# Performance work log

Measured on AMD Instinct MI355X. Metric: run time of the kernel, lower is better.

The kernel has to match this reference:

```python
import jax, jax.numpy as jnp
import numpy as np
from jax import lax

B = 32768
IMG = 28
K = 3
OUT_HW = IMG - K + 1  # 26
FLAT = OUT_HW * OUT_HW  # 676
HID = 300
NCLS = 10


def setup_inputs() -> dict:
    key = jax.random.key(0)
    ks = jax.random.split(key, 8)
    x = jax.random.normal(ks[0], (B, IMG * IMG), dtype=jnp.float32)
    conv_w = jax.random.normal(ks[1], (K, K), dtype=jnp.float32) * 0.1
    # Linear params stored as (in, out) so forward is h @ W + b
    W1 = jax.random.normal(ks[2], (FLAT, HID), dtype=jnp.float32) * 0.04
    b1 = jnp.zeros((HID,), dtype=jnp.float32)
    W2 = jax.random.normal(ks[3], (HID, HID), dtype=jnp.float32) * 0.06
    b2 = jnp.zeros((HID,), dtype=jnp.float32)
    W3 = jax.random.normal(ks[4], (HID, NCLS), dtype=jnp.float32) * 0.06
    b3 = jnp.zeros((NCLS,), dtype=jnp.float32)
    return {"x": x, "conv_w": conv_w, "W1": W1, "b1": b1,
            "W2": W2, "b2": b2, "W3": W3, "b3": b3}


def reference(x, conv_w, W1, b1, W2, b2, W3, b3):
    b = x.shape[0]
    img = x.reshape(b, 1, IMG, IMG)  # NCHW
    # Valid cross-correlation with 3x3 kernel -> [B,1,26,26]
    y = lax.conv_general_dilated(
        img, conv_w[None, None, :, :], window_strides=(1, 1), padding="VALID",
        dimension_numbers=("NCHW", "OIHW", "NCHW"))
    h = y.reshape(b, FLAT)
    h = jax.nn.relu(h @ W1 + b1)
    h = jax.nn.relu(h @ W2 + b2)
    return h @ W3 + b3
```

## Files before the change

kernel.cpp:

```cpp
#include <hip/hip_runtime.h>


typedef __bf16 bf16_t;
typedef __bf16 bf16x4 __attribute__((ext_vector_type(4)));
typedef __bf16 bf16x8 __attribute__((ext_vector_type(8)));
typedef float  f32x4  __attribute__((ext_vector_type(4)));

#define MFMA16(a, b, c) __builtin_amdgcn_mfma_f32_16x16x32_bf16((a), (b), (c), 0, 0, 0)

#define W1F_ELEMS (25 * 20 * 64 * 8)
#define W2F_ELEMS (10 * 20 * 64 * 8)
#define W3F_ELEMS (10 * 1 * 64 * 8)
#define ASTRIDE   136

#define W1F_GRP 32000
#define W2F_GRP 12800
#define W3F_GRP 640

#define WG_BARRIER_NODRAIN()                                   \
    do {                                                       \
        asm volatile("s_waitcnt lgkmcnt(0)" ::: "memory");     \
        __builtin_amdgcn_s_barrier();                          \
        __builtin_amdgcn_sched_barrier(0);                     \
    } while (0)

__global__ __launch_bounds__(256) void prep_weights(
    const float* __restrict__ conv_w, const float* __restrict__ W1,
    const float* __restrict__ W2, const float* __restrict__ W3,
    bf16x8* __restrict__ W1f, bf16x8* __restrict__ W2f,
    bf16x8* __restrict__ W3f) {
    int idx = blockIdx.x * 256 + threadIdx.x;
    if (idx < W1F_GRP) {
        int within = idx & 63, quad = within >> 4, nin = within & 15;
        int t = idx >> 6;
        int nt = t % 20, kcv = t / 20;
        int kb = kcv * 32 + quad * 8, n = nt * 16 + nin;
        bf16x8 vec;
#pragma unroll
        for (int j = 0; j < 8; ++j) {
            int k = kb + j;
            float v = 0.0f;
            if (k < 784 && n < 300) {
                int py = k / 28, px = k - py * 28;
#pragma unroll
                for (int ky = 0; ky < 3; ++ky) {
                    int oy = py - ky;
                    if (oy < 0 || oy > 25) continue;
#pragma unroll
                    for (int kx = 0; kx < 3; ++kx) {
                        int ox = px - kx;
                        if (ox < 0 || ox > 25) continue;
                        v += conv_w[ky * 3 + kx] * W1[(oy * 26 + ox) * 300 + n];
                    }
                }
            }
            vec[j] = (bf16_t)v;
        }
        W1f[idx] = vec;
    } else if (idx < W1F_GRP + W2F_GRP) {
        int g = idx - W1F_GRP;
        int within = g & 63, quad = within >> 4, nin = within & 15;
        int t = g >> 6;
        int nt = t % 20, kcv = t / 20;
        int kb = kcv * 32 + quad * 8, n = nt * 16 + nin;
        bf16x8 vec;
#pragma unroll
        for (int j = 0; j < 8; ++j) {
            int k = kb + j;
            vec[j] = (bf16_t)((k < 300 && n < 300) ? W2[k * 300 + n] : 0.0f);
        }
        W2f[g] = vec;
    } else if (idx < W1F_GRP + W2F_GRP + W3F_GRP) {
        int g = idx - (W1F_GRP + W2F_GRP);
        int within = g & 63, quad = within >> 4, n = within & 15;
        int kcv = g >> 6, kb = kcv * 32 + quad * 8;
        bf16x8 vec;
#pragma unroll
        for (int j = 0; j < 8; ++j) {
            int k = kb + j;
            vec[j] = (bf16_t)((k < 300 && n < 10) ? W3[k * 10 + n] : 0.0f);
        }
        W3f[g] = vec;
    }
}

__global__ __launch_bounds__(512, 4) void fused_mlp(
    const float* __restrict__ x, const float* __restrict__ b1,
    const float* __restrict__ b2, const float* __restrict__ b3,
    const bf16x8* __restrict__ W1f, const bf16x8* __restrict__ W2f,
    const bf16x8* __restrict__ W3f, float* __restrict__ out) {
    __shared__ bf16_t Abuf[2][64 * ASTRIDE];
    __shared__ bf16x8 hbuf[40 * 64];

    const int tid = threadIdx.x;
    const int w   = tid >> 6;
    const int l   = tid & 63;
    const int q   = l >> 4;
    const int l15 = l & 15;
    const int r0  = blockIdx.x * 64;

    const bool t3    = (w < 4);
    const int  nt0   = t3 ? (w * 3) : (12 + (w - 4) * 2);
    const int  boff2 = t3 ? 128 : 64;

    const int srow = tid >> 5;
    const int sc4  = tid & 31;
    const int trow = tid >> 3;
    const int tc4  = tid & 7;

    float4 pf[4];
#pragma unroll
    for (int i = 0; i < 4; ++i)
        pf[i] = *(const float4*)(x + (size_t)(r0 + i * 16 + srow) * 784 + sc4 * 4);

    f32x4 acc[4][3];
#pragma unroll
    for (int m = 0; m < 4; ++m)
#pragma unroll
        for (int j = 0; j < 3; ++j) acc[m][j] = (f32x4){0.f, 0.f, 0.f, 0.f};

    const bf16x8* bB1 = W1f + nt0 * 64 + l;

    int kc = 0;
    for (int band = 0; band < 7; ++band) {
        bf16_t* ab = Abuf[band & 1];

        if (band < 6) {
#pragma unroll
            for (int i = 0; i < 4; ++i) {
                bf16x4 v;
                v[0] = (bf16_t)pf[i].x; v[1] = (bf16_t)pf[i].y;
                v[2] = (bf16_t)pf[i].z; v[3] = (bf16_t)pf[i].w;
                *(bf16x4*)&ab[(i * 16 + srow) * ASTRIDE + sc4 * 4] = v;
            }
        } else {
            bf16x4 v;
            v[0] = (bf16_t)pf[0].x; v[1] = (bf16_t)pf[0].y;
            v[2] = (bf16_t)pf[0].z; v[3] = (bf16_t)pf[0].w;
            *(bf16x4*)&ab[trow * ASTRIDE + tc4 * 4] = v;
        }

        if (band + 1 < 6) {
#pragma unroll
            for (int i = 0; i < 4; ++i)
                pf[i] = *(const float4*)(x + (size_t)(r0 + i * 16 + srow) * 784 +
                                         (band + 1) * 128 + sc4 * 4);
        } else if (band + 1 == 6) {
            pf[0] = (tc4 < 4)
                ? *(const float4*)(x + (size_t)(r0 + trow) * 784 + 768 + tc4 * 4)
                : make_float4(0.f, 0.f, 0.f, 0.f);
        }

        WG_BARRIER_NODRAIN();

#define G1CHUNK(KCL)                                                            \
        {                                                                       \
            bf16x8 a0 = *(const bf16x8*)&ab[( 0 + l15) * ASTRIDE + (KCL) * 32 + q * 8]; \
            bf16x8 a1 = *(const bf16x8*)&ab[(16 + l15) * ASTRIDE + (KCL) * 32 + q * 8]; \
            bf16x8 a2 = *(const bf16x8*)&ab[(32 + l15) * ASTRIDE + (KCL) * 32 + q * 8]; \
            bf16x8 a3 = *(const bf16x8*)&ab[(48 + l15) * ASTRIDE + (KCL) * 32 + q * 8]; \
            const bf16x8* bp = bB1 + kc * 1280;                                 \
            bf16x8 b0 = bp[0], b1v = bp[64], b2v = bp[boff2];                   \
            acc[0][0] = MFMA16(a0, b0, acc[0][0]);                              \
            acc[1][0] = MFMA16(a1, b0, acc[1][0]);                              \
            acc[2][0] = MFMA16(a2, b0, acc[2][0]);                              \
            acc[3][0] = MFMA16(a3, b0, acc[3][0]);                              \
            acc[0][1] = MFMA16(a0, b1v, acc[0][1]);                             \
            acc[1][1] = MFMA16(a1, b1v, acc[1][1]);                             \
            acc[2][1] = MFMA16(a2, b1v, acc[2][1]);                             \
            acc[3][1] = MFMA16(a3, b1v, acc[3][1]);                             \
            if (t3) {                                                           \
                acc[0][2] = MFMA16(a0, b2v, acc[0][2]);                         \
                acc[1][2] = MFMA16(a1, b2v, acc[1][2]);                         \
                acc[2][2] = MFMA16(a2, b2v, acc[2][2]);                         \
                acc[3][2] = MFMA16(a3, b2v, acc[3][2]);                         \
            }                                                                   \
            ++kc;                                                               \
        }

        if (band < 6) {
            G1CHUNK(0) G1CHUNK(1) G1CHUNK(2) G1CHUNK(3)
        } else {
            G1CHUNK(0)
        }
    }

    bf16_t* hb = (bf16_t*)hbuf;

#define HSTORE(J, BIAS)                                                         \
    {                                                                           \
        int n = (nt0 + (J)) * 16 + l15;                                         \
        float bias = (n < 300) ? (BIAS)[n] : 0.0f;                              \
        int kh = n >> 5, quad = (n >> 3) & 3, jj = n & 7;                       \
        for (int mt = 0; mt < 4; ++mt)                                          \
            for (int r = 0; r < 4; ++r) {                                       \
                float v = acc[mt][(J)][r] + bias;                               \
                v = v > 0.f ? v : 0.f;                                          \
                hb[(((kh * 4 + mt) * 64 + quad * 16 + q * 4 + r) << 3) + jj] =  \
                    (bf16_t)v;                                                  \
            }                                                                   \
    }

    HSTORE(0, b1)
    HSTORE(1, b1)
    if (t3) HSTORE(2, b1)
    __syncthreads();

#pragma unroll
    for (int m = 0; m < 4; ++m)
#pragma unroll
        for (int j = 0; j < 3; ++j) acc[m][j] = (f32x4){0.f, 0.f, 0.f, 0.f};

    const bf16x8* bB2 = W2f + nt0 * 64 + l;

#define G2CHUNK(KC2)                                                            \
    {                                                                           \
        bf16x8 a0 = hbuf[((KC2) * 4 + 0) * 64 + l];                             \
        bf16x8 a1 = hbuf[((KC2) * 4 + 1) * 64 + l];                             \
        bf16x8 a2 = hbuf[((KC2) * 4 + 2) * 64 + l];                             \
        bf16x8 a3 = hbuf[((KC2) * 4 + 3) * 64 + l];                             \
        const bf16x8* bp = bB2 + (KC2) * 1280;                                  \
        bf16x8 b0 = bp[0], b1v = bp[64], b2v = bp[boff2];                       \
        acc[0][0] = MFMA16(a0, b0, acc[0][0]);                                  \
        acc[1][0] = MFMA16(a1, b0, acc[1][0]);                                  \
        acc[2][0] = MFMA16(a2, b0, acc[2][0]);                                  \
        acc[3][0] = MFMA16(a3, b0, acc[3][0]);                                  \
        acc[0][1] = MFMA16(a0, b1v, acc[0][1]);                                 \
        acc[1][1] = MFMA16(a1, b1v, acc[1][1]);                                 \
        acc[2][1] = MFMA16(a2, b1v, acc[2][1]);                                 \
        acc[3][1] = MFMA16(a3, b1v, acc[3][1]);                                 \
        if (t3) {                                                               \
            acc[0][2] = MFMA16(a0, b2v, acc[0][2]);                             \
            acc[1][2] = MFMA16(a1, b2v, acc[1][2]);                             \
            acc[2][2] = MFMA16(a2, b2v, acc[2][2]);                             \
            acc[3][2] = MFMA16(a3, b2v, acc[3][2]);                             \
        }                                                                       \
    }

    G2CHUNK(0) G2CHUNK(1) G2CHUNK(2) G2CHUNK(3) G2CHUNK(4)
    G2CHUNK(5) G2CHUNK(6) G2CHUNK(7) G2CHUNK(8) G2CHUNK(9)

    __syncthreads();

    HSTORE(0, b2)
    HSTORE(1, b2)
    if (t3) HSTORE(2, b2)
    __syncthreads();

    if (w < 4) {
        f32x4 acc3 = (f32x4){0.f, 0.f, 0.f, 0.f};
#pragma unroll
        for (int kc3 = 0; kc3 < 10; ++kc3)
            acc3 = MFMA16(hbuf[(kc3 * 4 + w) * 64 + l], W3f[kc3 * 64 + l], acc3);
        if (l15 < 10) {
            float bias = b3[l15];
#pragma unroll
            for (int r = 0; r < 4; ++r)
                out[(size_t)(r0 + w * 16 + q * 4 + r) * 10 + l15] = acc3[r] + bias;
        }
    }
}

extern "C" void kernel_launch(void* const* d_in, const int* in_sizes, int n_in,
                              void* d_out, int out_size, void* d_ws, size_t ws_size,
                              hipStream_t stream) {
    const float* x      = (const float*)d_in[0];
    const float* conv_w = (const float*)d_in[1];
    const float* W1     = (const float*)d_in[2];
    const float* b1     = (const float*)d_in[3];
    const float* W2     = (const float*)d_in[4];
    const float* b2     = (const float*)d_in[5];
    const float* W3     = (const float*)d_in[6];
    const float* b3     = (const float*)d_in[7];
    float* out = (float*)d_out;

    char* ws = (char*)d_ws;
    bf16_t* W1f = (bf16_t*)(ws);
    bf16_t* W2f = (bf16_t*)(ws + (size_t)W1F_ELEMS * 2);
    bf16_t* W3f = (bf16_t*)(ws + (size_t)(W1F_ELEMS + W2F_ELEMS) * 2);
    if (ws_size < (size_t)(W1F_ELEMS + W2F_ELEMS + W3F_ELEMS) * 2) return;

    int prep_total = W1F_GRP + W2F_GRP + W3F_GRP;
    prep_weights<<<(prep_total + 255) / 256, 256, 0, stream>>>(
        conv_w, W1, W2, W3, (bf16x8*)W1f, (bf16x8*)W2f, (bf16x8*)W3f);

    fused_mlp<<<32768 / 64, 512, 0, stream>>>(
        x, b1, b2, b3, (const bf16x8*)W1f, (const bf16x8*)W2f,
        (const bf16x8*)W3f, out);
}
```

Measured before the change: 194.7 us.

## Shrink fused MLP tile to 32 rows with 4 waves of 5 column tiles each

The fused MLP now processes 32 rows per 256-thread workgroup instead of 64 rows per 512 threads. Each wave owns five 16-column output tiles, which removes the uneven 3/2 tile split and its branch. The A staging buffer and the hidden buffer now share one aliased 20.8KB shared-memory array, the hidden buffer gets a padded stride to avoid bank conflicts, and plain syncthreads are replaced with non-draining barriers. The weight-prep kernel switches to one element per thread with scattered scalar stores. In exchange, each weight fragment loaded from global/L2 is reused across half as many rows, so weight traffic roughly doubles.

```diff
diff --git a/kernel.cpp b/kernel.cpp
--- a/kernel.cpp
+++ b/kernel.cpp
@@ -12,10 +12,7 @@
 #define W2F_ELEMS (10 * 20 * 64 * 8)
 #define W3F_ELEMS (10 * 1 * 64 * 8)
 #define ASTRIDE   136
-
-#define W1F_GRP 32000
-#define W2F_GRP 12800
-#define W3F_GRP 640
+#define HSTRIDE   65
 
 #define WG_BARRIER_NODRAIN()                                   \
     do {                                                       \
@@ -24,84 +21,72 @@
         __builtin_amdgcn_sched_barrier(0);                     \
     } while (0)
 
-__global__ __launch_bounds__(256) void prep_weights(
-    const float* __restrict__ conv_w, const float* __restrict__ W1,
-    const float* __restrict__ W2, const float* __restrict__ W3,
-    bf16x8* __restrict__ W1f, bf16x8* __restrict__ W2f,
-    bf16x8* __restrict__ W3f) {
+__global__ void prep_weights(const float* __restrict__ conv_w,
+                             const float* __restrict__ W1,
+                             const float* __restrict__ W2,
+                             const float* __restrict__ W3,
+                             bf16_t* __restrict__ W1f,
+                             bf16_t* __restrict__ W2f,
+                             bf16_t* __restrict__ W3f) {
     int idx = blockIdx.x * 256 + threadIdx.x;
-    if (idx < W1F_GRP) {
-        int within = idx & 63, quad = within >> 4, nin = within & 15;
-        int t = idx >> 6;
-        int nt = t % 20, kcv = t / 20;
-        int kb = kcv * 32 + quad * 8, n = nt * 16 + nin;
-        bf16x8 vec;
-#pragma unroll
-        for (int j = 0; j < 8; ++j) {
-            int k = kb + j;
-            float v = 0.0f;
-            if (k < 784 && n < 300) {
-                int py = k / 28, px = k - py * 28;
-#pragma unroll
-                for (int ky = 0; ky < 3; ++ky) {
-                    int oy = py - ky;
-                    if (oy < 0 || oy > 25) continue;
-#pragma unroll
-                    for (int kx = 0; kx < 3; ++kx) {
-                        int ox = px - kx;
-                        if (ox < 0 || ox > 25) continue;
-                        v += conv_w[ky * 3 + kx] * W1[(oy * 26 + ox) * 300 + n];
-                    }
+    if (idx < 800 * 320) {
+        int k = idx / 320;
+        int n = idx - k * 320;
+        float v = 0.0f;
+        if (k < 784 && n < 300) {
+            int py = k / 28;
+            int px = k - py * 28;
+#pragma unroll
+            for (int ky = 0; ky < 3; ++ky) {
+                int oy = py - ky;
+                if (oy < 0 || oy > 25) continue;
+#pragma unroll
+                for (int kx = 0; kx < 3; ++kx) {
+                    int ox = px - kx;
+                    if (ox < 0 || ox > 25) continue;
+                    v += conv_w[ky * 3 + kx] * W1[(oy * 26 + ox) * 300 + n];
                 }
             }
-            vec[j] = (bf16_t)v;
-        }
-        W1f[idx] = vec;
-    } else if (idx < W1F_GRP + W2F_GRP) {
-        int g = idx - W1F_GRP;
-        int within = g & 63, quad = within >> 4, nin = within & 15;
-        int t = g >> 6;
-        int nt = t % 20, kcv = t / 20;
-        int kb = kcv * 32 + quad * 8, n = nt * 16 + nin;
-        bf16x8 vec;
-#pragma unroll
-        for (int j = 0; j < 8; ++j) {
-            int k = kb + j;
-            vec[j] = (bf16_t)((k < 300 && n < 300) ? W2[k * 300 + n] : 0.0f);
-        }
-        W2f[g] = vec;
-    } else if (idx < W1F_GRP + W2F_GRP + W3F_GRP) {
-        int g = idx - (W1F_GRP + W2F_GRP);
-        int within = g & 63, quad = within >> 4, n = within & 15;
-        int kcv = g >> 6, kb = kcv * 32 + quad * 8;
-        bf16x8 vec;
-#pragma unroll
-        for (int j = 0; j < 8; ++j) {
-            int k = kb + j;
-            vec[j] = (bf16_t)((k < 300 && n < 10) ? W3[k * 10 + n] : 0.0f);
-        }
-        W3f[g] = vec;
+        }
+        int kc = k >> 5, quad = (k >> 3) & 3, j = k & 7;
+        int nt = n >> 4, nin = n & 15;
+        W1f[(((kc * 20 + nt) * 64 + quad * 16 + nin) << 3) + j] = (bf16_t)v;
+    } else if (idx < 800 * 320 + 320 * 320) {
+        int i2 = idx - 800 * 320;
+        int k = i2 / 320;
+        int n = i2 - k * 320;
+        float v = (k < 300 && n < 300) ? W2[k * 300 + n] : 0.0f;
+        int kc = k >> 5, quad = (k >> 3) & 3, j = k & 7;
+        int nt = n >> 4, nin = n & 15;
+        W2f[(((kc * 20 + nt) * 64 + quad * 16 + nin) << 3) + j] = (bf16_t)v;
+    } else if (idx < 800 * 320 + 320 * 320 + 320 * 16) {
+        int i3 = idx - (800 * 320 + 320 * 320);
+        int k = i3 / 16;
+        int n = i3 - k * 16;
+        float v = (k < 300 && n < 10) ? W3[k * 10 + n] : 0.0f;
+        int kc = k >> 5, quad = (k >> 3) & 3, j = k & 7;
+        W3f[(((kc * 64) + quad * 16 + n) << 3) + j] = (bf16_t)v;
     }
 }
 
-__global__ __launch_bounds__(512, 4) void fused_mlp(
+__global__ __launch_bounds__(256, 5) void fused_mlp(
     const float* __restrict__ x, const float* __restrict__ b1,
     const float* __restrict__ b2, const float* __restrict__ b3,
     const bf16x8* __restrict__ W1f, const bf16x8* __restrict__ W2f,
     const bf16x8* __restrict__ W3f, float* __restrict__ out) {
-    __shared__ bf16_t Abuf[2][64 * ASTRIDE];
-    __shared__ bf16x8 hbuf[40 * 64];
+    __shared__ __align__(16) unsigned char smem[20800];
+    bf16_t* AbufBase = (bf16_t*)smem;
+    bf16x8* hbuf     = (bf16x8*)smem;
+    bf16_t* hb       = (bf16_t*)smem;
 
     const int tid = threadIdx.x;
     const int w   = tid >> 6;
     const int l   = tid & 63;
     const int q   = l >> 4;
     const int l15 = l & 15;
-    const int r0  = blockIdx.x * 64;
-
-    const bool t3    = (w < 4);
-    const int  nt0   = t3 ? (w * 3) : (12 + (w - 4) * 2);
-    const int  boff2 = t3 ? 128 : 64;
+    const int r0  = blockIdx.x * 32;
+
+    const int nt0 = w * 5;
 
     const int srow = tid >> 5;
     const int sc4  = tid & 31;
@@ -111,19 +96,19 @@
     float4 pf[4];
 #pragma unroll
     for (int i = 0; i < 4; ++i)
-        pf[i] = *(const float4*)(x + (size_t)(r0 + i * 16 + srow) * 784 + sc4 * 4);
-
-    f32x4 acc[4][3];
-#pragma unroll
-    for (int m = 0; m < 4; ++m)
-#pragma unroll
-        for (int j = 0; j < 3; ++j) acc[m][j] = (f32x4){0.f, 0.f, 0.f, 0.f};
+        pf[i] = *(const float4*)(x + (size_t)(r0 + i * 8 + srow) * 784 + sc4 * 4);
+
+    f32x4 acc[2][5];
+#pragma unroll
+    for (int m = 0; m < 2; ++m)
+#pragma unroll
+        for (int j = 0; j < 5; ++j) acc[m][j] = (f32x4){0.f, 0.f, 0.f, 0.f};
 
     const bf16x8* bB1 = W1f + nt0 * 64 + l;
 
     int kc = 0;
     for (int band = 0; band < 7; ++band) {
-        bf16_t* ab = Abuf[band & 1];
+        bf16_t* ab = AbufBase + (band & 1) * (32 * ASTRIDE);
 
         if (band < 6) {
 #pragma unroll
@@ -131,7 +116,7 @@
                 bf16x4 v;
                 v[0] = (bf16_t)pf[i].x; v[1] = (bf16_t)pf[i].y;
                 v[2] = (bf16_t)pf[i].z; v[3] = (bf16_t)pf[i].w;
-                *(bf16x4*)&ab[(i * 16 + srow) * ASTRIDE + sc4 * 4] = v;
+                *(bf16x4*)&ab[(i * 8 + srow) * ASTRIDE + sc4 * 4] = v;
             }
         } else {
             bf16x4 v;
@@ -143,7 +128,7 @@
         if (band + 1 < 6) {
 #pragma unroll
             for (int i = 0; i < 4; ++i)
-                pf[i] = *(const float4*)(x + (size_t)(r0 + i * 16 + srow) * 784 +
+                pf[i] = *(const float4*)(x + (size_t)(r0 + i * 8 + srow) * 784 +
                                          (band + 1) * 128 + sc4 * 4);
         } else if (band + 1 == 6) {
             pf[0] = (tc4 < 4)
@@ -157,24 +142,19 @@
         {                                                                       \
             bf16x8 a0 = *(const bf16x8*)&ab[( 0 + l15) * ASTRIDE + (KCL) * 32 + q * 8]; \
             bf16x8 a1 = *(const bf16x8*)&ab[(16 + l15) * ASTRIDE + (KCL) * 32 + q * 8]; \
-            bf16x8 a2 = *(const bf16x8*)&ab[(32 + l15) * ASTRIDE + (KCL) * 32 + q * 8]; \
-            bf16x8 a3 = *(const bf16x8*)&ab[(48 + l15) * ASTRIDE + (KCL) * 32 + q * 8]; \
             const bf16x8* bp = bB1 + kc * 1280;                                 \
-            bf16x8 b0 = bp[0], b1v = bp[64], b2v = bp[boff2];                   \
+            bf16x8 b0 = bp[0], b1v = bp[64], b2v = bp[128];                     \
+            bf16x8 b3v = bp[192], b4v = bp[256];                                \
             acc[0][0] = MFMA16(a0, b0, acc[0][0]);                              \
             acc[1][0] = MFMA16(a1, b0, acc[1][0]);                              \
-            acc[2][0] = MFMA16(a2, b0, acc[2][0]);                              \
-            acc[3][0] = MFMA16(a3, b0, acc[3][0]);                              \
             acc[0][1] = MFMA16(a0, b1v, acc[0][1]);                             \
             acc[1][1] = MFMA16(a1, b1v, acc[1][1]);                             \
-            acc[2][1] = MFMA16(a2, b1v, acc[2][1]);                             \
-            acc[3][1] = MFMA16(a3, b1v, acc[3][1]);                             \
-            if (t3) {                                                           \
-                acc[0][2] = MFMA16(a0, b2v, acc[0][2]);                         \
-                acc[1][2] = MFMA16(a1, b2v, acc[1][2]);                         \
-                acc[2][2] = MFMA16(a2, b2v, acc[2][2]);                         \
-                acc[3][2] = MFMA16(a3, b2v, acc[3][2]);                         \
-            }                                                                   \
+            acc[0][2] = MFMA16(a0, b2v, acc[0][2]);                             \
+            acc[1][2] = MFMA16(a1, b2v, acc[1][2]);                             \
+            acc[0][3] = MFMA16(a0, b3v, acc[0][3]);                             \
+            acc[1][3] = MFMA16(a1, b3v, acc[1][3]);                             \
+            acc[0][4] = MFMA16(a0, b4v, acc[0][4]);                             \
+            acc[1][4] = MFMA16(a1, b4v, acc[1][4]);                             \
             ++kc;                                                               \
         }
 
@@ -185,73 +165,67 @@
         }
     }
 
-    bf16_t* hb = (bf16_t*)hbuf;
+    WG_BARRIER_NODRAIN();
 
 #define HSTORE(J, BIAS)                                                         \
     {                                                                           \
         int n = (nt0 + (J)) * 16 + l15;                                         \
         float bias = (n < 300) ? (BIAS)[n] : 0.0f;                              \
         int kh = n >> 5, quad = (n >> 3) & 3, jj = n & 7;                       \
-        for (int mt = 0; mt < 4; ++mt)                                          \
+        _Pragma("unroll")                                                       \
+        for (int mt = 0; mt < 2; ++mt)                                          \
+            _Pragma("unroll")                                                   \
             for (int r = 0; r < 4; ++r) {                                       \
                 float v = acc[mt][(J)][r] + bias;                               \
                 v = v > 0.f ? v : 0.f;                                          \
-                hb[(((kh * 4 + mt) * 64 + quad * 16 + q * 4 + r) << 3) + jj] =  \
-                    (bf16_t)v;                                                  \
+                hb[(((kh * 2 + mt) * HSTRIDE + quad * 16 + q * 4 + r) << 3) +   \
+                   jj] = (bf16_t)v;                                             \
             }                                                                   \
     }
 
-    HSTORE(0, b1)
-    HSTORE(1, b1)
-    if (t3) HSTORE(2, b1)
-    __syncthreads();
-
-#pragma unroll
-    for (int m = 0; m < 4; ++m)
-#pragma unroll
-        for (int j = 0; j < 3; ++j) acc[m][j] = (f32x4){0.f, 0.f, 0.f, 0.f};
+    HSTORE(0, b1) HSTORE(1, b1) HSTORE(2, b1) HSTORE(3, b1) HSTORE(4, b1)
+    WG_BARRIER_NODRAIN();
+
+#pragma unroll
+    for (int m = 0; m < 2; ++m)
+#pragma unroll
+        for (int j = 0; j < 5; ++j) acc[m][j] = (f32x4){0.f, 0.f, 0.f, 0.f};
 
     const bf16x8* bB2 = W2f + nt0 * 64 + l;
 
 #define G2CHUNK(KC2)                                                            \
     {                                                                           \
-        bf16x8 a0 = hbuf[((KC2) * 4 + 0) * 64 + l];                             \
-        bf16x8 a1 = hbuf[((KC2) * 4 + 1) * 64 + l];                             \
-        bf16x8 a2 = hbuf[((KC2) * 4 + 2) * 64 + l];                             \
-        bf16x8 a3 = hbuf[((KC2) * 4 + 3) * 64 + l];                             \
+        bf16x8 a0 = hbuf[((KC2) * 2 + 0) * HSTRIDE + l];                        \
+        bf16x8 a1 = hbuf[((KC2) * 2 + 1) * HSTRIDE + l];                        \
         const bf16x8* bp = bB2 + (KC2) * 1280;                                  \
-        bf16x8 b0 = bp[0], b1v = bp[64], b2v = bp[boff2];                       \
+        bf16x8 b0 = bp[0], b1v = bp[64], b2v = bp[128];                         \
+        bf16x8 b3v = bp[192], b4v = bp[256];                                    \
         acc[0][0] = MFMA16(a0, b0, acc[0][0]);                                  \
         acc[1][0] = MFMA16(a1, b0, acc[1][0]);                                  \
-        acc[2][0] = MFMA16(a2, b0, acc[2][0]);                                  \
-        acc[3][0] = MFMA16(a3, b0, acc[3][0]);                                  \
         acc[0][1] = MFMA16(a0, b1v, acc[0][1]);                                 \
         acc[1][1] = MFMA16(a1, b1v, acc[1][1]);                                 \
-        acc[2][1] = MFMA16(a2, b1v, acc[2][1]);                                 \
-        acc[3][1] = MFMA16(a3, b1v, acc[3][1]);                                 \
-        if (t3) {                                                               \
-            acc[0][2] = MFMA16(a0, b2v, acc[0][2]);                             \
-            acc[1][2] = MFMA16(a1, b2v, acc[1][2]);                             \
-            acc[2][2] = MFMA16(a2, b2v, acc[2][2]);                             \
-            acc[3][2] = MFMA16(a3, b2v, acc[3][2]);                             \
-        }                                                                       \
+        acc[0][2] = MFMA16(a0, b2v, acc[0][2]);                                 \
+        acc[1][2] = MFMA16(a1, b2v, acc[1][2]);                                 \
+        acc[0][3] = MFMA16(a0, b3v, acc[0][3]);                                 \
+        acc[1][3] = MFMA16(a1, b3v, acc[1][3]);                                 \
+        acc[0][4] = MFMA16(a0, b4v, acc[0][4]);                                 \
+        acc[1][4] = MFMA16(a1, b4v, acc[1][4]);                                 \
     }
 
     G2CHUNK(0) G2CHUNK(1) G2CHUNK(2) G2CHUNK(3) G2CHUNK(4)
     G2CHUNK(5) G2CHUNK(6) G2CHUNK(7) G2CHUNK(8) G2CHUNK(9)
 
-    __syncthreads();
-
-    HSTORE(0, b2)
-    HSTORE(1, b2)
-    if (t3) HSTORE(2, b2)
-    __syncthreads();
-
-    if (w < 4) {
+    WG_BARRIER_NODRAIN();
+
+    HSTORE(0, b2) HSTORE(1, b2) HSTORE(2, b2) HSTORE(3, b2) HSTORE(4, b2)
+    WG_BARRIER_NODRAIN();
+
+    if (w < 2) {
         f32x4 acc3 = (f32x4){0.f, 0.f, 0.f, 0.f};
 #pragma unroll
         for (int kc3 = 0; kc3 < 10; ++kc3)
-            acc3 = MFMA16(hbuf[(kc3 * 4 + w) * 64 + l], W3f[kc3 * 64 + l], acc3);
+            acc3 = MFMA16(hbuf[(kc3 * 2 + w) * HSTRIDE + l],
+                          W3f[kc3 * 64 + l], acc3);
         if (l15 < 10) {
             float bias = b3[l15];
 #pragma unroll
@@ -280,11 +254,11 @@
     bf16_t* W3f = (bf16_t*)(ws + (size_t)(W1F_ELEMS + W2F_ELEMS) * 2);
     if (ws_size < (size_t)(W1F_ELEMS + W2F_ELEMS + W3F_ELEMS) * 2) return;
 
-    int prep_total = W1F_GRP + W2F_GRP + W3F_GRP;
+    int prep_total = 800 * 320 + 320 * 320 + 320 * 16;
     prep_weights<<<(prep_total + 255) / 256, 256, 0, stream>>>(
-        conv_w, W1, W2, W3, (bf16x8*)W1f, (bf16x8*)W2f, (bf16x8*)W3f);
-
-    fused_mlp<<<32768 / 64, 512, 0, stream>>>(
+        conv_w, W1, W2, W3, W1f, W2f, W3f);
+
+    fused_mlp<<<32768 / 32, 256, 0, stream>>>(
         x, b1, b2, b3, (const bf16x8*)W1f, (const bf16x8*)W2f,
         (const bf16x8*)W3f, out);
 }
```

Result: no change. 196.7 us (+1.1%).
